# Performance work log

Measured on AMD Instinct MI355X. Metric: run time of the kernel, lower is better.

The kernel has to match this reference:

```python
import jax, jax.numpy as jnp
import numpy as np

B, T, D = 1, 2048, 2048
NH, DH, DRH, DC = 16, 128, 64, 512


def setup_inputs() -> dict:
    key = jax.random.key(0)
    ks = jax.random.split(key, 12)
    p = lambda k, s: jax.random.normal(k, s, jnp.float32) * 0.02
    h = jax.random.normal(ks[0], (B, T, D), jnp.float32)
    # rotation angles; reference builds complex freqs_cis = cos + i*sin
    freqs_cis = jax.random.uniform(ks[1], (T, DRH // 2), jnp.float32, 0.0, 2.0 * np.pi)
    causal = jnp.tril(jnp.ones((T, T), bool))
    mask = jnp.where(causal, 0.0, -1e9).astype(jnp.float32)
    return {
        "h": h,
        "freqs_cis": freqs_cis,
        "mask": mask,
        "w_dkv": p(ks[2], (DC, D)),
        "w_uk": p(ks[3], (DH, NH, DC)),
        "w_uv": p(ks[4], (DH, NH, DC)),
        "w_dq": p(ks[5], (DC, D)),
        "w_uq": p(ks[6], (DH, NH, DC)),
        "w_qr": p(ks[7], (DRH, NH, DC)),
        "w_kr": p(ks[8], (DRH, D)),
        "w_o": p(ks[9], (D, DH, NH)),
    }


def _rope(x, fc):
    # x: [..., t, drh]; fc: complex [t, drh//2] (broadcasts over leading dims)
    real, imag = jnp.split(x.astype(jnp.float32), 2, -1)
    z = (real + 1j * imag) * fc
    return jnp.concatenate((z.real, z.imag), -1).astype(x.dtype)


def reference(h, freqs_cis, mask, w_dkv, w_uk, w_uv, w_dq, w_uq, w_qr, w_kr, w_o):
    nh, dh, drh = w_uk.shape[1], w_uk.shape[0], w_qr.shape[0]
    fc = jnp.cos(freqs_cis) + 1j * jnp.sin(freqs_cis)  # [t, drh//2] complex
    c_kv = jnp.einsum('cd,btd->btc', w_dkv, h)          # kv latent [b,t,dc]
    k_c = jnp.einsum('enc,btc->bnte', w_uk, c_kv)       # [b,nh,t,dh]
    v_c = jnp.einsum('enc,btc->bnte', w_uv, c_kv)       # [b,nh,t,dh]
    c_q = jnp.einsum('cd,btd->btc', w_dq, h)            # q latent [b,t,dc]
    q_c = jnp.einsum('enc,btc->bnte', w_uq, c_q)        # [b,nh,t,dh]
    q_r = _rope(jnp.einsum('rnc,btc->bntr', w_qr, c_q), fc)  # [b,nh,t,drh]
    k_r = _rope(jnp.einsum('rd,btd->btr', w_kr, h), fc)      # [b,t,drh]
    q = jnp.concatenate((q_c, q_r), -1)                 # [b,nh,t,dh+drh]
    b, t = k_r.shape[0], k_r.shape[1]
    k_r = jnp.broadcast_to(k_r[:, None], (b, nh, t, drh)) / nh
    k = jnp.concatenate((k_c, k_r), -1)                 # [b,nh,t,dh+drh]
    logits = jnp.einsum('bntd,bnld->bntl', q, k) / jnp.sqrt(jnp.float32(dh + drh)) + mask
    scores = jax.nn.softmax(logits.astype(jnp.float32), -1).astype(h.dtype)
    # NOTE: faithful to source: contraction is over the query axis t, output axis is l
    out = jnp.einsum('bntl,bnte->bnle', scores, v_c)    # [b,nh,t,dh] (t named l in src)
    return jnp.einsum('den,bnle->bld', w_o, out)        # [b,t,d]
```

## Files before the change

### kernel.cpp

```cpp
#include <hip/hip_runtime.h>
#include <hip/hip_bf16.h>
#include <math.h>


namespace {

constexpr int T   = 2048;
constexpr int D   = 2048;
constexpr int NH  = 16;
constexpr int DH  = 128;
constexpr int DRH = 64;
constexpr int DC  = 512;
constexpr int QK  = 192;
constexpr float SCL2E = 0.07216878364870322f * 1.4426950408889634f;

constexpr long long PH = 2048LL * 32 * 33;

typedef __attribute__((ext_vector_type(8))) short short8;
typedef __attribute__((ext_vector_type(4))) float f32x4;

#define MFMA16(a, b, c) __builtin_amdgcn_mfma_f32_16x16x32_bf16((a), (b), (c), 0, 0, 0)

__device__ __forceinline__ unsigned short f2b(float x) {
    unsigned u = __float_as_uint(x);
    unsigned r = (u + 0x7FFFu + ((u >> 16) & 1u)) >> 16;
    return (unsigned short)r;
}
__device__ __forceinline__ unsigned short f2bt(float x) {
    return (unsigned short)(__float_as_uint(x) >> 16);
}
__device__ __forceinline__ float b2f(unsigned short s) {
    return __uint_as_float(((unsigned)s) << 16);
}

typedef __attribute__((address_space(1))) const unsigned int* gas_t;
typedef __attribute__((address_space(3))) unsigned int* las_t;
__device__ __forceinline__ void async16(const unsigned short* g, unsigned short* l) {
    __builtin_amdgcn_global_load_lds((gas_t)(const void*)g, (las_t)(void*)l, 16, 0, 0);
}

constexpr long long SZ_H    = (long long)T * D;
constexpr long long SZ_DKV  = (long long)DC * D;
constexpr long long SZ_UK   = (long long)DH * NH * DC;
constexpr long long SZ_UV   = SZ_UK;
constexpr long long SZ_DQ   = SZ_DKV;
constexpr long long SZ_UQ   = SZ_UK;
constexpr long long SZ_QR   = (long long)DRH * NH * DC;
constexpr long long SZ_KR   = (long long)DRH * D;
constexpr long long C0 = SZ_H;
constexpr long long C1 = C0 + SZ_DKV;
constexpr long long C2 = C1 + SZ_UK;
constexpr long long C3 = C2 + SZ_UV;
constexpr long long C4 = C3 + SZ_DQ;
constexpr long long C5 = C4 + SZ_UQ;
constexpr long long C6 = C5 + SZ_QR;
constexpr long long C7 = C6 + SZ_KR;
constexpr long long C8 = C7 + 32768;

__global__ __launch_bounds__(256) void cast_all(
    const float* __restrict__ h,   const float* __restrict__ wdkv,
    const float* __restrict__ wuk, const float* __restrict__ wuv,
    const float* __restrict__ wdq, const float* __restrict__ wuq,
    const float* __restrict__ wqr, const float* __restrict__ wkr,
    unsigned short* __restrict__ hb,   unsigned short* __restrict__ dkvb,
    unsigned short* __restrict__ dqb,  unsigned short* __restrict__ ukvb,
    unsigned short* __restrict__ wqall, unsigned short* __restrict__ krb,
    float* __restrict__ zrow)
{
    long long i4 = ((long long)blockIdx.x * 256 + threadIdx.x) * 4;
    const float* src; unsigned short* dst; long long soff, doff;
    if      (i4 < C0) { src = h;    dst = hb;   soff = i4;      doff = soff; }
    else if (i4 < C1) { src = wdkv; dst = dkvb; soff = i4 - C0; doff = soff; }
    else if (i4 < C2) {
        src = wuk; dst = ukvb; soff = i4 - C1;
        long long e = soff >> 13, n = (soff >> 9) & 15, c = soff & 511;
        doff = n * 131072 + e * 512 + c;
    }
    else if (i4 < C3) {
        src = wuv; dst = ukvb; soff = i4 - C2;
        long long e = soff >> 13, n = (soff >> 9) & 15, c = soff & 511;
        doff = n * 131072 + (128 + e) * 512 + c;
    }
    else if (i4 < C4) { src = wdq;  dst = dqb;  soff = i4 - C3; doff = soff; }
    else if (i4 < C5) {
        src = wuq; dst = wqall; soff = i4 - C4;
        long long e = soff >> 13, n = (soff >> 9) & 15, c = soff & 511;
        doff = n * 98304 + e * 512 + c;
    }
    else if (i4 < C6) {
        src = wqr; dst = wqall; soff = i4 - C5;
        long long e = soff >> 13, n = (soff >> 9) & 15, c = soff & 511;
        doff = n * 98304 + (128 + e) * 512 + c;
    }
    else if (i4 < C7) { src = wkr;  dst = krb;  soff = i4 - C6; doff = soff; }
    else {
        float4 z4; z4.x = 0.f; z4.y = 0.f; z4.z = 0.f; z4.w = 0.f;
        *(float4*)(zrow + (i4 - C7)) = z4;
        return;
    }
    float4 v = *(const float4*)(src + soff);
    uint2 pk;
    pk.x = (unsigned)f2b(v.x) | ((unsigned)f2b(v.y) << 16);
    pk.y = (unsigned)f2b(v.z) | ((unsigned)f2b(v.w) << 16);
    *(uint2*)(dst + doff) = pk;
}

__global__ __launch_bounds__(256) void wo_permute(const float* __restrict__ wo,
                                                  unsigned short* __restrict__ wob)
{
    __shared__ float row[2048];
    int d = blockIdx.x;
    const float* src = wo + (long long)d * 2048;
#pragma unroll
    for (int i = 0; i < 8; ++i) row[threadIdx.x + i * 256] = src[threadIdx.x + i * 256];
    __syncthreads();
    unsigned short* dst = wob + (long long)d * 2048;
#pragma unroll
    for (int i = 0; i < 8; ++i) {
        int j = threadIdx.x + i * 256;
        int n = j >> 7, e = j & 127;
        dst[j] = f2b(row[e * 16 + n]);
    }
}

template<int BM, int BN, int WM, int WN, bool OUTB, bool SPLITK = false, bool MERGEKV = false>
__global__ __launch_bounds__(256) void gemm_bf16(
    const unsigned short* __restrict__ A, const unsigned short* __restrict__ B,
    void* __restrict__ C, int K, int lda, int ldb, int ldc,
    long long sB, long long sC,
    void* __restrict__ C2, int ldc2, long long sC2)
{
    constexpr int MT = WM / 16, NT = WN / 16;
    constexpr int WX = BN / WN;
    __shared__ unsigned short As[2][BM * 32];
    __shared__ unsigned short Bs[2][BN * 32];
    const int tid = (int)threadIdx.x;
    const int wave = tid >> 6, lane = tid & 63;
    const int q = lane >> 4, c = lane & 15;
    const int wm = (wave / WX) * WM, wn = (wave % WX) * WN;
    const int m0 = (int)blockIdx.x * BM, n0 = (int)blockIdx.y * BN;

    const unsigned short* Ab;
    const unsigned short* Bb;
    long long cb;
    void* Cp = C;
    int ldcl = ldc;
    int n0c = n0;
    if constexpr (SPLITK) {
        int koff = (int)blockIdx.z * K;
        Ab = A + koff;
        Bb = B + koff;
        cb = (long long)blockIdx.z * sC;
    } else {
        Ab = A;
        Bb = B + (long long)blockIdx.z * sB;
        cb = (long long)blockIdx.z * sC;
    }
    if constexpr (MERGEKV) {
        if (blockIdx.y == 1) {
            Cp = C2; ldcl = ldc2; n0c = 0;
            cb = (long long)blockIdx.z * sC2;
        }
    }

    f32x4 acc[MT][NT];
#pragma unroll
    for (int i = 0; i < MT; ++i)
#pragma unroll
        for (int j = 0; j < NT; ++j) acc[i][j] = (f32x4){0.f, 0.f, 0.f, 0.f};

    auto STAGE = [&](int buf, int k0) {
#pragma unroll
        for (int i = 0; i < BM / 64; ++i) {
            int ch = tid + i * 256;
            async16(&Ab[(long long)(m0 + (ch >> 2)) * lda + k0 + (((ch & 3) ^ ((ch >> 3) & 3)) * 8)],
                    &As[buf][(i * 256 + wave * 64) * 8]);
        }
#pragma unroll
        for (int i = 0; i < BN / 64; ++i) {
            int ch = tid + i * 256;
            async16(&Bb[(long long)(n0 + (ch >> 2)) * ldb + k0 + (((ch & 3) ^ ((ch >> 3) & 3)) * 8)],
                    &Bs[buf][(i * 256 + wave * 64) * 8]);
        }
    };

    STAGE(0, 0);
    __syncthreads();
    int cur = 0;
    for (int k0 = 0; k0 < K; k0 += 32) {
        if (k0 + 32 < K) STAGE(cur ^ 1, k0 + 32);
        short8 af[MT], bfr[NT];
#pragma unroll
        for (int i = 0; i < MT; ++i) {
            int row = wm + i * 16 + c;
            af[i] = *(const short8*)&As[cur][row * 32 + (q ^ ((row >> 1) & 3)) * 8];
        }
#pragma unroll
        for (int j = 0; j < NT; ++j) {
            int row = wn + j * 16 + c;
            bfr[j] = *(const short8*)&Bs[cur][row * 32 + (q ^ ((row >> 1) & 3)) * 8];
        }
#pragma unroll
        for (int i = 0; i < MT; ++i)
#pragma unroll
            for (int j = 0; j < NT; ++j)
                acc[i][j] = MFMA16(af[i], bfr[j], acc[i][j]);
        __syncthreads();
        cur ^= 1;
    }
#pragma unroll
    for (int i = 0; i < MT; ++i)
#pragma unroll
        for (int j = 0; j < NT; ++j) {
            int rbase = m0 + wm + i * 16 + q * 4;
            int col = n0c + wn + j * 16 + c;
#pragma unroll
            for (int rr = 0; rr < 4; ++rr) {
                long long off = cb + (long long)(rbase + rr) * ldcl + col;
                if (OUTB) ((unsigned short*)Cp)[off] = f2b(acc[i][j][rr]);
                else      ((float*)Cp)[off] = acc[i][j][rr];
            }
        }
}

__global__ __launch_bounds__(256) void rope_qk(unsigned short* __restrict__ qh,
                                               const float* __restrict__ krtp,
                                               unsigned short* __restrict__ kh,
                                               const float* __restrict__ fr)
{
    int idx = (int)blockIdx.x * 256 + (int)threadIdx.x;
    if (idx < NH * T * 32) {
        int j = idx & 31;
        int t = (idx >> 5) & (T - 1);
        int n = idx >> 16;
        float sn, cs;
        sincosf(fr[t * 32 + j], &sn, &cs);
        long long base = ((long long)(n * T + t)) * QK + 128 + j;
        float x0 = b2f(qh[base]);
        float x1 = b2f(qh[base + 32]);
        qh[base]      = f2b(x0 * cs - x1 * sn);
        qh[base + 32] = f2b(x0 * sn + x1 * cs);
    } else {
        idx -= NH * T * 32;
        int j = idx & 31;
        int t = idx >> 5;
        float sn, cs;
        sincosf(fr[t * 32 + j], &sn, &cs);
        float x0 = 0.f, x1 = 0.f;
#pragma unroll
        for (int pth = 0; pth < 4; ++pth) {
            x0 += krtp[pth * (T * 64) + t * 64 + j];
            x1 += krtp[pth * (T * 64) + t * 64 + 32 + j];
        }
        unsigned short y0 = f2b((x0 * cs - x1 * sn) * (1.0f / 16.0f));
        unsigned short y1 = f2b((x0 * sn + x1 * cs) * (1.0f / 16.0f));
#pragma unroll
        for (int n = 0; n < NH; ++n) {
            long long base = ((long long)(n * T + t)) * QK + 128 + j;
            kh[base]      = y0;
            kh[base + 32] = y1;
        }
    }
}

__global__ __launch_bounds__(256) void vtrans(const unsigned short* __restrict__ vbh,
                                              const float* __restrict__ zrow,
                                              unsigned short* __restrict__ vt)
{
    __shared__ unsigned short ts[32][33];
    __shared__ float zi[32];
    int t0 = (int)blockIdx.x * 32, e0 = (int)blockIdx.y * 32, n = (int)blockIdx.z;
    int tid = (int)threadIdx.x;
    if (tid < 32) zi[tid] = 1.0f / zrow[n * T + t0 + tid];
    int r = tid >> 3, cq = (tid & 7) * 4;
    const unsigned short* src = vbh + ((long long)(n * T + t0 + r)) * DH + e0 + cq;
#pragma unroll
    for (int i = 0; i < 4; ++i) ts[r][cq + i] = src[i];
    __syncthreads();
    unsigned short* dst = vt + ((long long)(n * DH + e0 + r)) * T + t0 + cq;
#pragma unroll
    for (int i = 0; i < 4; ++i) dst[i] = f2b(b2f(ts[cq + i][r]) * zi[cq + i]);
}

__global__ __launch_bounds__(256) void row_stats_p(const unsigned short* __restrict__ qh,
                                                   const unsigned short* __restrict__ kh,
                                                   float* __restrict__ zrow,
                                                   unsigned short* __restrict__ Pbuf)
{
    int id = (int)blockIdx.x;
    int n = (id & 7) * 2 + ((id >> 3) & 1);
    int rest = id >> 4;
    int tbi = 31 - (rest & 31);
    int chunk = rest >> 5;
    int tid = (int)threadIdx.x, wave = tid >> 6, lane = tid & 63;
    int q = lane >> 4, c = lane & 15;
    int tw = tbi * 64 + wave * 16;

    __shared__ unsigned short Ks[64 * 200];

    const unsigned short* qp = qh + ((long long)(n * T + tw + c)) * QK;
    short8 qf[6];
#pragma unroll
    for (int f = 0; f < 6; ++f) qf[f] = *(const short8*)(qp + f * 32 + q * 8);

    float z = 0.f;
    const unsigned short* kbase = kh + (long long)n * T * QK;
    unsigned short* Ph = Pbuf + (long long)n * PH;

    short8 kreg[6];
    int lt = chunk;
    if (lt <= tbi) {
        const unsigned short* kp = kbase + (long long)lt * 64 * QK;
#pragma unroll
        for (int i = 0; i < 6; ++i) {
            int ch = tid + i * 256;
            int r = ch / 24, cc = ch - r * 24;
            kreg[i] = *(const short8*)(kp + r * QK + cc * 8);
        }
    }
    for (; lt <= tbi; lt += 4) {
        __syncthreads();
#pragma unroll
        for (int i = 0; i < 6; ++i) {
            int ch = tid + i * 256;
            int r = ch / 24, cc = ch - r * 24;
            *(short8*)&Ks[r * 200 + cc * 8] = kreg[i];
        }
        __syncthreads();
        if (lt + 4 <= tbi) {
            const unsigned short* kp = kbase + (long long)(lt + 4) * 64 * QK;
#pragma unroll
            for (int i = 0; i < 6; ++i) {
                int ch = tid + i * 256;
                int r = ch / 24, cc = ch - r * 24;
                kreg[i] = *(const short8*)(kp + r * QK + cc * 8);
            }
        }
        f32x4 d[4];
#pragma unroll
        for (int ls = 0; ls < 4; ++ls) d[ls] = (f32x4){0.f, 0.f, 0.f, 0.f};
        __builtin_amdgcn_s_setprio(1);
#pragma unroll
        for (int f = 0; f < 6; ++f)
#pragma unroll
            for (int ls = 0; ls < 4; ++ls) {
                short8 ka = *(const short8*)&Ks[(ls * 16 + c) * 200 + f * 32 + q * 8];
                d[ls] = MFMA16(ka, qf[f], d[ls]);
            }
        __builtin_amdgcn_s_setprio(0);
        int L = T - lt * 64;
        unsigned short* pb = Ph + (long long)2048 * lt * (65 - lt)
                             + (long long)(q * 4) * L + (tbi - lt) * 64 + wave * 16 + c;
        if (lt == tbi) {
            int tl = wave * 16 + c;
#pragma unroll
            for (int ls = 0; ls < 4; ++ls)
#pragma unroll
                for (int r = 0; r < 4; ++r) {
                    float pe = exp2f(d[ls][r] * SCL2E);
                    bool ok = (ls * 16 + q * 4 + r) <= tl;
                    z += ok ? pe : 0.f;
                    pb[(ls * 16 + r) * L] = ok ? f2bt(pe) : (unsigned short)0;
                }
        } else {
#pragma unroll
            for (int ls = 0; ls < 4; ++ls)
#pragma unroll
                for (int r = 0; r < 4; ++r) {
                    float pe = exp2f(d[ls][r] * SCL2E);
                    z += pe;
                    pb[(ls * 16 + r) * L] = f2bt(pe);
                }
        }
    }
    z += __shfl_xor(z, 16);
    z += __shfl_xor(z, 32);
    if (q == 0) atomicAdd(&zrow[n * T + tw + c], z);
}

__global__ __launch_bounds__(256) void pv_gemm(const unsigned short* __restrict__ Pbuf,
                                               const unsigned short* __restrict__ vt,
                                               unsigned short* __restrict__ p0,
                                               unsigned short* __restrict__ p1)
{
    __shared__ unsigned short As[2][64 * 32];
    __shared__ unsigned short Bs[2][128 * 32];
    int id = (int)blockIdx.x;
    int n = (id & 7) * 2 + ((id >> 3) & 1);
    int rest = id >> 4;
    int pr = rest & 15;
    int chunk = (rest >> 4) & 1;
    const int tid = (int)threadIdx.x, wave = tid >> 6, lane = tid & 63;
    const int q = lane >> 4, c = lane & 15;
    const int wm = (wave >> 1) * 32, wn = (wave & 1) * 64;
    unsigned short* op = chunk ? p1 : p0;

#pragma unroll
    for (int ph = 0; ph < 2; ++ph) {
        int j = ph ? (31 - pr) : pr;
        int m0 = j * 64;
        int L = T - m0;
        int ntile = 32 - j;
        const unsigned short* A = Pbuf + (long long)n * PH + (long long)2048 * j * (65 - j);
        const unsigned short* B = vt + (long long)n * DH * T + m0;

        f32x4 acc[2][4];
#pragma unroll
        for (int i = 0; i < 2; ++i)
#pragma unroll
            for (int jj = 0; jj < 4; ++jj) acc[i][jj] = (f32x4){0.f, 0.f, 0.f, 0.f};

        int tcnt = (chunk < ntile) ? (((ntile - 1 - chunk) >> 1) + 1) : 0;
        int nsteps = tcnt * 2;

        auto STAGE = [&](int buf, int k0) {
            async16(&A[(long long)(tid >> 2) * L + k0 + (((tid & 3) ^ ((tid >> 3) & 3)) * 8)],
                    &As[buf][wave * 512]);
#pragma unroll
            for (int i = 0; i < 2; ++i) {
                int ch = tid + i * 256;
                async16(&B[(long long)(ch >> 2) * T + k0 + (((ch & 3) ^ ((ch >> 3) & 3)) * 8)],
                        &Bs[buf][(i * 256 + wave * 64) * 8]);
            }
        };
        auto K0 = [&](int s) { return (chunk + ((s >> 1) << 1)) * 64 + (s & 1) * 32; };

        if (nsteps > 0) STAGE(0, K0(0));
        __syncthreads();
        int cur = 0;
        for (int s = 0; s < nsteps; ++s) {
            if (s + 1 < nsteps) STAGE(cur ^ 1, K0(s + 1));
            short8 af[2], bfr[4];
#pragma unroll
            for (int i = 0; i < 2; ++i) {
                int row = wm + i * 16 + c;
                af[i] = *(const short8*)&As[cur][row * 32 + (q ^ ((row >> 1) & 3)) * 8];
            }
#pragma unroll
            for (int jj = 0; jj < 4; ++jj) {
                int row = wn + jj * 16 + c;
                bfr[jj] = *(const short8*)&Bs[cur][row * 32 + (q ^ ((row >> 1) & 3)) * 8];
            }
#pragma unroll
            for (int i = 0; i < 2; ++i)
#pragma unroll
                for (int jj = 0; jj < 4; ++jj)
                    acc[i][jj] = MFMA16(af[i], bfr[jj], acc[i][jj]);
            __syncthreads();
            cur ^= 1;
        }
#pragma unroll
        for (int i = 0; i < 2; ++i)
#pragma unroll
            for (int jj = 0; jj < 4; ++jj) {
                int rbase = m0 + wm + i * 16 + q * 4;
                int col = n * 128 + wn + jj * 16 + c;
#pragma unroll
                for (int rr = 0; rr < 4; ++rr)
                    op[(long long)(rbase + rr) * D + col] = f2b(acc[i][jj][rr]);
            }
    }
}

__global__ __launch_bounds__(256) void sum_cast2(const unsigned short* a,
                                                 const unsigned short* b,
                                                 unsigned short* o)
{
    long long i = ((long long)blockIdx.x * 256 + threadIdx.x) * 8;
    short8 va = *(const short8*)(a + i);
    short8 vb = *(const short8*)(b + i);
    short8 vo;
#pragma unroll
    for (int j = 0; j < 8; ++j)
        vo[j] = (short)f2b(b2f((unsigned short)va[j]) + b2f((unsigned short)vb[j]));
    *(short8*)(o + i) = vo;
}

}

extern "C" void kernel_launch(void* const* d_in, const int* in_sizes, int n_in,
                              void* d_out, int out_size, void* d_ws, size_t ws_size,
                              hipStream_t stream)
{
    (void)in_sizes; (void)n_in; (void)out_size; (void)ws_size;
    const float* h    = (const float*)d_in[0];
    const float* fr   = (const float*)d_in[1];
    const float* wdkv = (const float*)d_in[3];
    const float* wuk  = (const float*)d_in[4];
    const float* wuv  = (const float*)d_in[5];
    const float* wdq  = (const float*)d_in[6];
    const float* wuq  = (const float*)d_in[7];
    const float* wqr  = (const float*)d_in[8];
    const float* wkr  = (const float*)d_in[9];
    const float* wo   = (const float*)d_in[10];
    float* out = (float*)d_out;

    char* p = (char*)d_ws;
    auto alloc = [&](long long bytes) { char* r = p; p += (bytes + 255) & ~255LL; return r; };
    unsigned short* qhb   = (unsigned short*)alloc((long long)NH * T * QK * 2);
    unsigned short* khb   = (unsigned short*)alloc((long long)NH * T * QK * 2);
    unsigned short* vbh   = (unsigned short*)alloc((long long)NH * T * DH * 2);
    float*          zrow  = (float*)alloc((long long)NH * T * 4);
    unsigned short* vtb   = (unsigned short*)alloc((long long)NH * T * DH * 2);
    unsigned short* Pbuf  = (unsigned short*)alloc(PH * NH * 2);
    char* q = (char*)Pbuf;
    auto sub = [&](long long bytes) { char* r = q; q += (bytes + 255) & ~255LL; return r; };
    unsigned short* hb    = (unsigned short*)sub(SZ_H * 2);
    unsigned short* dkvb  = (unsigned short*)sub(SZ_DKV * 2);
    unsigned short* dqb   = (unsigned short*)sub(SZ_DQ * 2);
    unsigned short* ukvb  = (unsigned short*)sub((SZ_UK + SZ_UV) * 2);
    unsigned short* wqall = (unsigned short*)sub((SZ_UQ + SZ_QR) * 2);
    unsigned short* krb   = (unsigned short*)sub(SZ_KR * 2);
    unsigned short* ckvq  = (unsigned short*)sub((long long)T * 1024 * 2);
    float*          krt   = (float*)sub((long long)T * DRH * 4 * 4);
    unsigned short* pvp0  = qhb;
    unsigned short* pvp1  = khb;
    unsigned short* attn2 = pvp0;
    unsigned short* wob   = vtb;

    cast_all<<<dim3((unsigned)(C8 / 1024)), 256, 0, stream>>>(
        h, wdkv, wuk, wuv, wdq, wuq, wqr, wkr, hb, dkvb, dqb, ukvb, wqall, krb, zrow);

    gemm_bf16<64,64,32,32,true><<<dim3(T/64, 1024/64, 1), 256, 0, stream>>>(
        hb, dkvb, ckvq, D, D, D, 1024, 0, 0, nullptr, 0, 0);
    gemm_bf16<64,64,32,32,false,true><<<dim3(T/64, 1, 4), 256, 0, stream>>>(
        hb, krb, krt, D/4, D, D, DRH, 0, (long long)T * DRH, nullptr, 0, 0);
    gemm_bf16<64,128,32,64,true,false,true><<<dim3(T/64, 2, NH), 256, 0, stream>>>(
        ckvq, ukvb, khb, DC, 1024, DC, QK, (long long)256 * DC, (long long)T * QK,
        vbh, DH, (long long)T * DH);
    gemm_bf16<128,64,32,64,true><<<dim3(T/128, 3, NH), 256, 0, stream>>>(
        ckvq + DC, wqall, qhb, DC, 1024, DC, QK, (long long)192 * DC, (long long)T * QK,
        nullptr, 0, 0);

    rope_qk<<<dim3((NH * T * 32 + T * 32) / 256), 256, 0, stream>>>(qhb, krt, khb, fr);

    row_stats_p<<<dim3(2048), 256, 0, stream>>>(qhb, khb, zrow, Pbuf);
    vtrans<<<dim3(T/32, DH/32, NH), 256, 0, stream>>>(vbh, zrow, vtb);
    pv_gemm<<<dim3(512), 256, 0, stream>>>(Pbuf, vtb, pvp0, pvp1);
    sum_cast2<<<dim3(T * D / 2048), 256, 0, stream>>>(pvp0, pvp1, attn2);

    wo_permute<<<dim3(D), 256, 0, stream>>>(wo, wob);
    gemm_bf16<64,128,32,64,false><<<dim3(T/64, D/128, 1), 256, 0, stream>>>(
        attn2, wob, out, D, D, D, D, 0, 0, nullptr, 0, 0);
}
```

Baseline: 304.8 us.

## Triple-buffer GEMM LDS staging with vmcnt waits and merge epilogue prep kernels

Moves the bf16 GEMM and PV GEMM main loops from double to triple LDS buffering. Loads are issued two steps ahead, and the full __syncthreads is replaced by explicit s_waitcnt vmcnt counts plus a raw s_barrier, so more global-to-LDS traffic is in flight. It also fuses the W_o permute/cast and the partial-sum cast into a single launch to save one kernel dispatch. In exchange it uses more LDS per block, which may lower occupancy, and correctness now depends on the hand-counted vmcnt values matching the number of loads issued per stage.

```diff
diff --git a/kernel.cpp b/kernel.cpp
--- a/kernel.cpp
+++ b/kernel.cpp
@@ -37,6 +37,14 @@
 typedef __attribute__((address_space(3))) unsigned int* las_t;
 __device__ __forceinline__ void async16(const unsigned short* g, unsigned short* l) {
     __builtin_amdgcn_global_load_lds((gas_t)(const void*)g, (las_t)(void*)l, 16, 0, 0);
+}
+
+template<int N>
+__device__ __forceinline__ void vmwait() {
+    if constexpr (N == 0)      asm volatile("s_waitcnt vmcnt(0)" ::: "memory");
+    else if constexpr (N == 2) asm volatile("s_waitcnt vmcnt(2)" ::: "memory");
+    else if constexpr (N == 3) asm volatile("s_waitcnt vmcnt(3)" ::: "memory");
+    else static_assert(N == 0 || N == 2 || N == 3, "add vmcnt case");
 }
 
 constexpr long long SZ_H    = (long long)T * D;
@@ -105,24 +113,6 @@
     *(uint2*)(dst + doff) = pk;
 }
 
-__global__ __launch_bounds__(256) void wo_permute(const float* __restrict__ wo,
-                                                  unsigned short* __restrict__ wob)
-{
-    __shared__ float row[2048];
-    int d = blockIdx.x;
-    const float* src = wo + (long long)d * 2048;
-#pragma unroll
-    for (int i = 0; i < 8; ++i) row[threadIdx.x + i * 256] = src[threadIdx.x + i * 256];
-    __syncthreads();
-    unsigned short* dst = wob + (long long)d * 2048;
-#pragma unroll
-    for (int i = 0; i < 8; ++i) {
-        int j = threadIdx.x + i * 256;
-        int n = j >> 7, e = j & 127;
-        dst[j] = f2b(row[e * 16 + n]);
-    }
-}
-
 template<int BM, int BN, int WM, int WN, bool OUTB, bool SPLITK = false, bool MERGEKV = false>
 __global__ __launch_bounds__(256) void gemm_bf16(
     const unsigned short* __restrict__ A, const unsigned short* __restrict__ B,
@@ -132,8 +122,9 @@
 {
     constexpr int MT = WM / 16, NT = WN / 16;
     constexpr int WX = BN / WN;
-    __shared__ unsigned short As[2][BM * 32];
-    __shared__ unsigned short Bs[2][BN * 32];
+    constexpr int LOADS = BM / 64 + BN / 64;
+    __shared__ unsigned short As[3][BM * 32];
+    __shared__ unsigned short Bs[3][BN * 32];
     const int tid = (int)threadIdx.x;
     const int wave = tid >> 6, lane = tid & 63;
     const int q = lane >> 4, c = lane & 15;
@@ -184,11 +175,14 @@
         }
     };
 
+    const int nsteps = K >> 5;
     STAGE(0, 0);
-    __syncthreads();
-    int cur = 0;
-    for (int k0 = 0; k0 < K; k0 += 32) {
-        if (k0 + 32 < K) STAGE(cur ^ 1, k0 + 32);
+    if (nsteps > 1) { STAGE(1, 32); vmwait<LOADS>(); }
+    else vmwait<0>();
+    __builtin_amdgcn_s_barrier();
+    for (int s = 0; s < nsteps; ++s) {
+        int cur = s % 3;
+        if (s + 2 < nsteps) STAGE((s + 2) % 3, (s + 2) * 32);
         short8 af[MT], bfr[NT];
 #pragma unroll
         for (int i = 0; i < MT; ++i) {
@@ -205,8 +199,11 @@
 #pragma unroll
             for (int j = 0; j < NT; ++j)
                 acc[i][j] = MFMA16(af[i], bfr[j], acc[i][j]);
-        __syncthreads();
-        cur ^= 1;
+        if (s + 1 < nsteps) {
+            if (s + 2 < nsteps) vmwait<LOADS>();
+            else vmwait<0>();
+            __builtin_amdgcn_s_barrier();
+        }
     }
 #pragma unroll
     for (int i = 0; i < MT; ++i)
@@ -383,8 +380,8 @@
                                                unsigned short* __restrict__ p0,
                                                unsigned short* __restrict__ p1)
 {
-    __shared__ unsigned short As[2][64 * 32];
-    __shared__ unsigned short Bs[2][128 * 32];
+    __shared__ unsigned short As[3][64 * 32];
+    __shared__ unsigned short Bs[3][128 * 32];
     int id = (int)blockIdx.x;
     int n = (id & 7) * 2 + ((id >> 3) & 1);
     int rest = id >> 4;
@@ -425,11 +422,15 @@
         };
         auto K0 = [&](int s) { return (chunk + ((s >> 1) << 1)) * 64 + (s & 1) * 32; };
 
-        if (nsteps > 0) STAGE(0, K0(0));
-        __syncthreads();
-        int cur = 0;
+        if (nsteps > 0) {
+            STAGE(0, K0(0));
+            if (nsteps > 1) { STAGE(1, K0(1)); vmwait<3>(); }
+            else vmwait<0>();
+        }
+        __builtin_amdgcn_s_barrier();
         for (int s = 0; s < nsteps; ++s) {
-            if (s + 1 < nsteps) STAGE(cur ^ 1, K0(s + 1));
+            int cur = s % 3;
+            if (s + 2 < nsteps) STAGE((s + 2) % 3, K0(s + 2));
             short8 af[2], bfr[4];
 #pragma unroll
             for (int i = 0; i < 2; ++i) {
@@ -446,8 +447,11 @@
 #pragma unroll
                 for (int jj = 0; jj < 4; ++jj)
                     acc[i][jj] = MFMA16(af[i], bfr[jj], acc[i][jj]);
-            __syncthreads();
-            cur ^= 1;
+            if (s + 1 < nsteps) {
+                if (s + 2 < nsteps) vmwait<3>();
+                else vmwait<0>();
+                __builtin_amdgcn_s_barrier();
+            }
         }
 #pragma unroll
         for (int i = 0; i < 2; ++i)
@@ -459,21 +463,40 @@
                 for (int rr = 0; rr < 4; ++rr)
                     op[(long long)(rbase + rr) * D + col] = f2b(acc[i][jj][rr]);
             }
-    }
-}
-
-__global__ __launch_bounds__(256) void sum_cast2(const unsigned short* a,
-                                                 const unsigned short* b,
-                                                 unsigned short* o)
-{
-    long long i = ((long long)blockIdx.x * 256 + threadIdx.x) * 8;
-    short8 va = *(const short8*)(a + i);
-    short8 vb = *(const short8*)(b + i);
-    short8 vo;
-#pragma unroll
-    for (int j = 0; j < 8; ++j)
-        vo[j] = (short)f2b(b2f((unsigned short)va[j]) + b2f((unsigned short)vb[j]));
-    *(short8*)(o + i) = vo;
+        __builtin_amdgcn_s_barrier();
+    }
+}
+
+__global__ __launch_bounds__(256) void epilogue_prep(const float* __restrict__ wo,
+                                                     unsigned short* __restrict__ wob,
+                                                     const unsigned short* a,
+                                                     const unsigned short* b,
+                                                     unsigned short* o)
+{
+    __shared__ float row[2048];
+    int bid = (int)blockIdx.x;
+    if (bid < D) {
+        const float* src = wo + (long long)bid * 2048;
+#pragma unroll
+        for (int i = 0; i < 8; ++i) row[threadIdx.x + i * 256] = src[threadIdx.x + i * 256];
+        __syncthreads();
+        unsigned short* dst = wob + (long long)bid * 2048;
+#pragma unroll
+        for (int i = 0; i < 8; ++i) {
+            int j = threadIdx.x + i * 256;
+            int n = j >> 7, e = j & 127;
+            dst[j] = f2b(row[e * 16 + n]);
+        }
+    } else {
+        long long i = ((long long)(bid - D) * 256 + threadIdx.x) * 8;
+        short8 va = *(const short8*)(a + i);
+        short8 vb = *(const short8*)(b + i);
+        short8 vo;
+#pragma unroll
+        for (int j = 0; j < 8; ++j)
+            vo[j] = (short)f2b(b2f((unsigned short)va[j]) + b2f((unsigned short)vb[j]));
+        *(short8*)(o + i) = vo;
+    }
 }
 
 }
@@ -537,9 +560,9 @@
     row_stats_p<<<dim3(2048), 256, 0, stream>>>(qhb, khb, zrow, Pbuf);
     vtrans<<<dim3(T/32, DH/32, NH), 256, 0, stream>>>(vbh, zrow, vtb);
     pv_gemm<<<dim3(512), 256, 0, stream>>>(Pbuf, vtb, pvp0, pvp1);
-    sum_cast2<<<dim3(T * D / 2048), 256, 0, stream>>>(pvp0, pvp1, attn2);
-
-    wo_permute<<<dim3(D), 256, 0, stream>>>(wo, wob);
+
+    epilogue_prep<<<dim3(D + T * D / 2048), 256, 0, stream>>>(wo, wob, pvp0, pvp1, attn2);
+
     gemm_bf16<64,128,32,64,false><<<dim3(T/64, D/128, 1), 256, 0, stream>>>(
         attn2, wob, out, D, D, D, D, 0, 0, nullptr, 0, 0);
 }
```

After: 310.5 us. No clear change (+1.9%).
